# Performance work log

Hardware: AMD Instinct MI355X
Metric: run time of the kernel (lower is better)

The kernel has to match this reference:

```python
import jax, jax.numpy as jnp
import numpy as np

EPS = 1e-5


def setup_inputs() -> dict:
    key = jax.random.key(0)
    ks = jax.random.split(key, 6)
    B, N, F = 8, 8192, 64
    xyzs = jax.random.uniform(ks[0], (B, N, 3), dtype=jnp.float32)
    feats = jax.random.normal(ks[1], (B, N, F), dtype=jnp.float32)
    c_in = 3 + F  # 67
    dims = [(64, c_in), (64, 64), (128, 64)]
    inp = {"xyzs": xyzs, "feats": feats}
    for i, (co, ci) in enumerate(dims, start=1):
        inp[f"w{i}"] = jax.random.normal(ks[1 + i], (co, ci), dtype=jnp.float32) / np.sqrt(ci)
        inp[f"b{i}"] = jnp.zeros((co,), jnp.float32)
        inp[f"g{i}"] = jnp.ones((co,), jnp.float32)
        inp[f"bt{i}"] = jnp.zeros((co,), jnp.float32)
        inp[f"m{i}"] = jnp.zeros((co,), jnp.float32)
        inp[f"v{i}"] = jnp.ones((co,), jnp.float32)
    return inp


def sample_farthest_points(xyz, S):
    # Iterative FPS starting from index 0 (pytorch3d default random_start_point=False).
    B, N, _ = xyz.shape
    barange = jnp.arange(B)

    def step(carry, _):
        mind, last = carry                      # mind: [B,N] min sq-dist to selected set
        lastp = xyz[barange, last]              # [B,3]
        d = jnp.sum((xyz - lastp[:, None, :]) ** 2, -1)
        mind = jnp.minimum(mind, d)
        nxt = jnp.argmax(mind, axis=1).astype(jnp.int32)
        return (mind, nxt), nxt

    init = (jnp.full((B, N), 1e10, xyz.dtype), jnp.zeros((B,), jnp.int32))
    _, rest = jax.lax.scan(step, init, None, length=S - 1)  # [S-1, B]
    idx = jnp.concatenate([jnp.zeros((1, B), jnp.int32), rest], 0).T  # [B,S]
    return xyz[barange[:, None], idx], idx


def ball_query(centers, xyz, K, radius):
    # First-K-in-radius semantics of pytorch3d.ops.ball_query; pad idx with -1,
    # pad gathered points with zeros (masked_gather behavior).
    B, N, _ = xyz.shape
    d2 = (jnp.sum(centers ** 2, -1)[:, :, None]
          + jnp.sum(xyz ** 2, -1)[:, None, :]
          - 2.0 * jnp.einsum('bsd,bnd->bsn', centers, xyz))  # [B,S,N]
    within = d2 <= radius * radius
    skey = jnp.where(within, jnp.arange(N, dtype=jnp.int32), N)
    negvals, idx = jax.lax.top_k(-skey, K)      # K smallest keys = first K in-radius
    valid = (-negvals) < N                       # [B,S,K]
    group_idx = jnp.where(valid, idx, -1)
    gathered = xyz[jnp.arange(B)[:, None, None], jnp.where(valid, idx, 0)]  # [B,S,K,3]
    group_xyz = jnp.where(valid[..., None], gathered, 0.0)
    return group_idx, group_xyz


def _mlp_layer(x, w, b, g, bt, m, v):
    # 1x1 Conv2d over channel axis + BatchNorm (eval stats) + ReLU; x: [B,S,K,Cin]
    y = jnp.einsum('bskc,oc->bsko', x, w) + b
    y = g * (y - m) * jax.lax.rsqrt(v + EPS) + bt
    return jax.nn.relu(y)


def reference(xyzs, feats, w1, b1, g1, bt1, m1, v1,
              w2, b2, g2, bt2, m2, v2, w3, b3, g3, bt3, m3, v3):
    S, K, radius = 2048, 32, 0.2
    B = xyzs.shape[0]
    center_xyzs, _ = sample_farthest_points(xyzs, S)             # [B,S,3]
    group_idxs, group_xyzs = ball_query(center_xyzs, xyzs, K, radius)
    group_xyzs = group_xyzs - center_xyzs[:, :, None, :]          # relative coords
    batch_idxs = jnp.arange(B)[:, None, None]
    gf = feats[batch_idxs, jnp.where(group_idxs < 0, 0, group_idxs)]  # [B,S,K,F]
    gf = jnp.concatenate([group_xyzs, gf], axis=-1)
    gf = gf * (group_idxs != -1)[..., None].astype(gf.dtype)      # zero padded slots
    x = _mlp_layer(gf, w1, b1, g1, bt1, m1, v1)
    x = _mlp_layer(x, w2, b2, g2, bt2, m2, v2)
    x = _mlp_layer(x, w3, b3, g3, bt3, m3, v3)
    center_feats = jnp.max(x, axis=2)                             # max over neighbors
    return center_xyzs, center_feats
```

## Files before the change

### kernel.cpp

```cpp
#include <hip/hip_runtime.h>


#define NPTS 8192
#define SCTR 2048
#define NB   8
#define KNN  32
#define NF   64
#define WT_FLOATS (67*64 + 64*64 + 64*128)
#define PROG_STRIDE 32

typedef float v2f __attribute__((ext_vector_type(2)));

__device__ __forceinline__ v2f fps_sqdist_v2(v2f px, v2f py, v2f pz,
                                             v2f lx, v2f ly, v2f lz) {
#pragma clang fp contract(off)
  v2f dx = px - lx;
  v2f dy = py - ly;
  v2f dz = pz - lz;
  v2f xx = dx * dx;
  v2f yy = dy * dy;
  v2f zz = dz * dz;
  return (xx + yy) + zz;
}

__device__ __forceinline__ float sumsq3(float x, float y, float z) {
#pragma clang fp contract(off)
  return (x * x + y * y) + z * z;
}

__device__ __forceinline__ float bq_d2(float sc, float sx,
                                       float cx, float cy, float cz,
                                       float x, float y, float z) {
#pragma clang fp contract(off)
  float dt = fmaf(cz, z, fmaf(cy, y, cx * x));
  return (sc + sx) - 2.0f * dt;
}

template <int CTRL>
__device__ __forceinline__ unsigned long long kmax_dpp(unsigned long long k) {
  int lo = (int)(unsigned int)(k & 0xFFFFFFFFull);
  int hi = (int)(unsigned int)(k >> 32);
  int slo = __builtin_amdgcn_update_dpp(lo, lo, CTRL, 0xF, 0xF, false);
  int shi = __builtin_amdgcn_update_dpp(hi, hi, CTRL, 0xF, 0xF, false);
  unsigned long long sk =
      ((unsigned long long)(unsigned int)shi << 32) | (unsigned int)slo;
  return sk > k ? sk : k;
}

template <int CTRL>
__device__ __forceinline__ void kmax_dpp_pay(unsigned long long& k,
                                             float& x, float& y, float& z) {
  int lo = (int)(unsigned int)(k & 0xFFFFFFFFull);
  int hi = (int)(unsigned int)(k >> 32);
  int slo = __builtin_amdgcn_update_dpp(lo, lo, CTRL, 0xF, 0xF, false);
  int shi = __builtin_amdgcn_update_dpp(hi, hi, CTRL, 0xF, 0xF, false);
  int sx  = __builtin_amdgcn_update_dpp(__float_as_int(x), __float_as_int(x), CTRL, 0xF, 0xF, false);
  int sy  = __builtin_amdgcn_update_dpp(__float_as_int(y), __float_as_int(y), CTRL, 0xF, 0xF, false);
  int sz  = __builtin_amdgcn_update_dpp(__float_as_int(z), __float_as_int(z), CTRL, 0xF, 0xF, false);
  unsigned long long sk =
      ((unsigned long long)(unsigned int)shi << 32) | (unsigned int)slo;
  if (sk > k) {
    k = sk;
    x = __int_as_float(sx);
    y = __int_as_float(sy);
    z = __int_as_float(sz);
  }
}

__global__ __launch_bounds__(256) void init_kernel(
    const float* __restrict__ w1, const float* __restrict__ w2,
    const float* __restrict__ w3, float* __restrict__ wT,
    int* __restrict__ prog)
{
  const int t = threadIdx.x;
  if (blockIdx.x == 0 && t < NB) prog[t * PROG_STRIDE] = 0;
  int idx = blockIdx.x * 256 + t;
  if (idx < 67*64) {
    int c = idx >> 6, o = idx & 63;
    wT[idx] = w1[o*67 + c];
  } else if (idx < 67*64 + 64*64) {
    int r = idx - 67*64; int c = r >> 6, o = r & 63;
    wT[idx] = w2[o*64 + c];
  } else if (idx < 67*64 + 64*64 + 64*128) {
    int r = idx - (67*64 + 64*64); int c = r >> 7, o = r & 127;
    wT[idx] = w3[o*64 + c];
  }
}

__global__ __launch_bounds__(256, 1) void mega_kernel(
    const float* __restrict__ xyzs, const float* __restrict__ feats,
    float* centers, const float* __restrict__ wT, int* prog,
    const float* __restrict__ b1, const float* __restrict__ g1, const float* __restrict__ bt1,
    const float* __restrict__ m1, const float* __restrict__ v1,
    const float* __restrict__ b2, const float* __restrict__ g2, const float* __restrict__ bt2,
    const float* __restrict__ m2, const float* __restrict__ v2,
    const float* __restrict__ b3, const float* __restrict__ g3, const float* __restrict__ bt3,
    const float* __restrict__ m3, const float* __restrict__ v3,
    float* out_feats)
{
  __shared__ __align__(16) float smem[8784];

  if (blockIdx.x < NB) {
    __builtin_amdgcn_s_setprio(3);
    const int b = blockIdx.x;
    const int t = threadIdx.x;
    const int t4 = 4 * t;
    const float* xb = xyzs + (size_t)b * NPTS * 3;
    int* prog_b = prog + b * PROG_STRIDE;
    float* cb_ = centers + (size_t)b * SCTR * 3;

#define LOADQ(QX, QY, QZ, QOFF)                                               \
    { const float4* p_ = (const float4*)(xb + (size_t)3 * ((QOFF) + t4));     \
      float4 l0 = p_[0], l1 = p_[1], l2 = p_[2];                              \
      QX = make_float4(l0.x, l0.w, l1.z, l2.y);                               \
      QY = make_float4(l0.y, l1.x, l1.w, l2.z);                               \
      QZ = make_float4(l0.z, l1.y, l2.x, l2.w); }

    float4 xA, yA, zA, xB, yB, zB, xC, yC, zC, xD, yD, zD;
    float4 xE, yE, zE, xF, yF, zF, xG, yG, zG, xH, yH, zH;
    LOADQ(xA, yA, zA, 0);
    LOADQ(xB, yB, zB, 1024);
    LOADQ(xC, yC, zC, 2048);
    LOADQ(xD, yD, zD, 3072);
    LOADQ(xE, yE, zE, 4096);
    LOADQ(xF, yF, zF, 5120);
    LOADQ(xG, yG, zG, 6144);
    LOADQ(xH, yH, zH, 7168);
#undef LOADQ

    float4 mA = make_float4(1e10f, 1e10f, 1e10f, 1e10f);
    float4 mB = mA, mC = mA, mD = mA, mE = mA, mF = mA, mG = mA, mH = mA;

    if (t == 0) { smem[0] = xA.x; smem[1] = yA.x; smem[2] = zA.x; }
    __syncthreads();
    float lx = smem[0], ly = smem[1], lz = smem[2];
    if (t == 0) { cb_[0] = lx; cb_[1] = ly; cb_[2] = lz; }

#define FPS_QUAD(QX, QY, QZ, MV, QOFF, BV, BG)                                  \
  do {                                                                          \
    v2f d;                                                                      \
    d = fps_sqdist_v2((v2f){QX.x,QX.y}, (v2f){QY.x,QY.y}, (v2f){QZ.x,QZ.y},     \
                      lxv, lyv, lzv);                                           \
    MV.x = fminf(MV.x, d.x); if (MV.x > BV) { BV = MV.x; BG = (QOFF)+t4+0; }    \
    MV.y = fminf(MV.y, d.y); if (MV.y > BV) { BV = MV.y; BG = (QOFF)+t4+1; }    \
    d = fps_sqdist_v2((v2f){QX.z,QX.w}, (v2f){QY.z,QY.w}, (v2f){QZ.z,QZ.w},     \
                      lxv, lyv, lzv);                                           \
    MV.z = fminf(MV.z, d.x); if (MV.z > BV) { BV = MV.z; BG = (QOFF)+t4+2; }    \
    MV.w = fminf(MV.w, d.y); if (MV.w > BV) { BV = MV.w; BG = (QOFF)+t4+3; }    \
  } while (0)

    for (int s = 1; s < SCTR; ++s) {
      float bv0 = -1.0f, bv1 = -1.0f; int bg0 = 0, bg1 = 0;
      {
        v2f lxv = {lx, lx}, lyv = {ly, ly}, lzv = {lz, lz};
        FPS_QUAD(xA, yA, zA, mA, 0,    bv0, bg0);
        FPS_QUAD(xB, yB, zB, mB, 1024, bv0, bg0);
        FPS_QUAD(xC, yC, zC, mC, 2048, bv0, bg0);
        FPS_QUAD(xD, yD, zD, mD, 3072, bv0, bg0);
        FPS_QUAD(xE, yE, zE, mE, 4096, bv1, bg1);
        FPS_QUAD(xF, yF, zF, mF, 5120, bv1, bg1);
        FPS_QUAD(xG, yG, zG, mG, 6144, bv1, bg1);
        FPS_QUAD(xH, yH, zH, mH, 7168, bv1, bg1);
      }
      float bv = bv0; int bg = bg0;
      if (bv1 > bv0) { bv = bv1; bg = bg1; }

      unsigned long long key =
          ((unsigned long long)__float_as_uint(bv) << 13) |
          (unsigned long long)(8191 - bg);

      key = kmax_dpp<0x111>(key);
      key = kmax_dpp<0x112>(key);
      key = kmax_dpp<0x114>(key);
      key = kmax_dpp<0x118>(key);
      key = kmax_dpp<0x142>(key);
      key = kmax_dpp<0x143>(key);
      int skl = __builtin_amdgcn_readlane((int)(unsigned int)(key & 0xFFFFFFFFull), 63);
      int skh = __builtin_amdgcn_readlane((int)(unsigned int)(key >> 32), 63);
      int widx = 8191 - (skl & 0x1FFF);
      int q = widx >> 10;
      int j = widx & 3;
      int othr = (widx & 1023) >> 2;
      float wx = 0.f, wy = 0.f, wz = 0.f;
      if (t == othr) {
        float4 qx, qy, qz;
        switch (q) {
          case 0: qx = xA; qy = yA; qz = zA; break;
          case 1: qx = xB; qy = yB; qz = zB; break;
          case 2: qx = xC; qy = yC; qz = zC; break;
          case 3: qx = xD; qy = yD; qz = zD; break;
          case 4: qx = xE; qy = yE; qz = zE; break;
          case 5: qx = xF; qy = yF; qz = zF; break;
          case 6: qx = xG; qy = yG; qz = zG; break;
          default: qx = xH; qy = yH; qz = zH; break;
        }
        wx = (j == 0) ? qx.x : ((j == 1) ? qx.y : ((j == 2) ? qx.z : qx.w));
        wy = (j == 0) ? qy.x : ((j == 1) ? qy.y : ((j == 2) ? qy.z : qy.w));
        wz = (j == 0) ? qz.x : ((j == 1) ? qz.y : ((j == 2) ? qz.z : qz.w));
      }
      int ol = othr & 63;
      wx = __int_as_float(__builtin_amdgcn_readlane(__float_as_int(wx), ol));
      wy = __int_as_float(__builtin_amdgcn_readlane(__float_as_int(wy), ol));
      wz = __int_as_float(__builtin_amdgcn_readlane(__float_as_int(wz), ol));

      int pb = s & 1;
      if ((t & 63) == 63) {
        float* slot = smem + (size_t)((pb * 4 + (t >> 6)) * 8);
        slot[0] = __int_as_float(skl);
        slot[1] = __int_as_float(skh);
        slot[2] = wx; slot[3] = wy; slot[4] = wz;
      }
      __syncthreads();
      const float* rs = smem + (size_t)((pb * 4 + (t & 3)) * 8);
      unsigned long long k4 =
          ((unsigned long long)(unsigned int)__float_as_int(rs[1]) << 32) |
          (unsigned int)__float_as_int(rs[0]);
      float px = rs[2], py = rs[3], pz = rs[4];
      kmax_dpp_pay<0xB1>(k4, px, py, pz);
      kmax_dpp_pay<0x4E>(k4, px, py, pz);
      lx = px; ly = py; lz = pz;

      if (t == 0) {
        float* o = cb_ + 3 * s;
        o[0] = lx; o[1] = ly; o[2] = lz;
        if ((s & 31) == 31)
          __hip_atomic_store(prog_b, s + 1, __ATOMIC_RELEASE, __HIP_MEMORY_SCOPE_AGENT);
      }
    }
#undef FPS_QUAD
    return;
  }

  constexpr float R2 = (float)(0.2 * 0.2);
  const int t    = threadIdx.x;
  const int jb   = blockIdx.x - NB;
  const int half = t >> 7;
  const int ht   = t & 127;
  const int w    = ht >> 6;
  const int lane = ht & 63;
  const int cid  = 2 * jb + half;
  const int b    = cid & 7;
  const int s    = cid >> 3;
  const int bid  = b * SCTR + s;
  const float* xb = xyzs + (size_t)b * NPTS * 3;

  float* in_  = smem + half * 4352;
  float* y_   = in_ + 2176;
  int*   gidx = (int*)(smem + 8704) + half * KNN;
  float* csl  = smem + 8768 + half * 4;

  if (ht == 0) {
    int* pb_ = prog + b * PROG_STRIDE;
    while (__hip_atomic_load(pb_, __ATOMIC_RELAXED, __HIP_MEMORY_SCOPE_AGENT) <= s)
      __builtin_amdgcn_s_sleep(64);
    const int* cg = (const int*)(centers + (size_t)bid * 3);
    csl[0] = __int_as_float(__hip_atomic_load(cg + 0, __ATOMIC_RELAXED, __HIP_MEMORY_SCOPE_AGENT));
    csl[1] = __int_as_float(__hip_atomic_load(cg + 1, __ATOMIC_RELAXED, __HIP_MEMORY_SCOPE_AGENT));
    csl[2] = __int_as_float(__hip_atomic_load(cg + 2, __ATOMIC_RELAXED, __HIP_MEMORY_SCOPE_AGENT));
  }
  __syncthreads();
  const float cx = csl[0], cy = csl[1], cz = csl[2];
  const float sc = sumsq3(cx, cy, cz);

  int cnt = 0;
  for (int base = 0; base < NPTS && cnt < KNN; base += 64) {
    int n = base + lane;
    float x = xb[n*3+0], y = xb[n*3+1], z = xb[n*3+2];
    float sx = sumsq3(x, y, z);
    float d2 = bq_d2(sc, sx, cx, cy, cz, x, y, z);
    bool within = (d2 <= R2);
    unsigned long long mk = __ballot(within);
    int rank = __popcll(mk & ((1ull << lane) - 1ull));
    int slot = cnt + rank;
    if (within && slot < KNN) gidx[slot] = n;
    cnt += (int)__popcll(mk);
  }
  if (cnt > KNN) cnt = KNN;
  __syncthreads();

#pragma unroll 4
  for (int k2 = 0; k2 < 16; ++k2) {
    int k = 2*k2 + w;
    int gk = (k < cnt) ? gidx[k] : -1;
    float fv = 0.f, xv = 0.f;
    if (gk >= 0) {
      fv = feats[((size_t)b * NPTS + gk) * NF + lane];
      if (lane < 3) xv = xb[gk*3 + lane] - csl[lane];
    }
    in_[k*68 + 3 + lane] = fv;
    if (lane < 3) in_[k*68 + lane] = xv;
    if (lane == 3) in_[k*68 + 67] = 0.f;
  }
  __syncthreads();

  const int g  = lane >> 3;
  const int h  = lane & 7;
  const int ob = w*32 + 4*h;
  const float* w1T = wT;
  const float* w2T = wT + 67*64;
  const float* w3T = wT + 67*64 + 64*64;

#define FMA_COL(AS0, AS1, AS2, AS3, WV)                                      \
  do {                                                                       \
    acc[0][0]=fmaf(AS0, WV.x, acc[0][0]); acc[0][1]=fmaf(AS0, WV.y, acc[0][1]); \
    acc[0][2]=fmaf(AS0, WV.z, acc[0][2]); acc[0][3]=fmaf(AS0, WV.w, acc[0][3]); \
    acc[1][0]=fmaf(AS1, WV.x, acc[1][0]); acc[1][1]=fmaf(AS1, WV.y, acc[1][1]); \
    acc[1][2]=fmaf(AS1, WV.z, acc[1][2]); acc[1][3]=fmaf(AS1, WV.w, acc[1][3]); \
    acc[2][0]=fmaf(AS2, WV.x, acc[2][0]); acc[2][1]=fmaf(AS2, WV.y, acc[2][1]); \
    acc[2][2]=fmaf(AS2, WV.z, acc[2][2]); acc[2][3]=fmaf(AS2, WV.w, acc[2][3]); \
    acc[3][0]=fmaf(AS3, WV.x, acc[3][0]); acc[3][1]=fmaf(AS3, WV.y, acc[3][1]); \
    acc[3][2]=fmaf(AS3, WV.z, acc[3][2]); acc[3][3]=fmaf(AS3, WV.w, acc[3][3]); \
  } while (0)

#define MLP_CHUNK(SRC, WBASE, WSTRIDE, WOFF)                                 \
  do {                                                                       \
    float4 a0 = *(const float4*)((SRC) + (4*g+0)*68 + c0);                   \
    float4 a1 = *(const float4*)((SRC) + (4*g+1)*68 + c0);                   \
    float4 a2 = *(const float4*)((SRC) + (4*g+2)*68 + c0);                   \
    float4 a3 = *(const float4*)((SRC) + (4*g+3)*68 + c0);                   \
    float4 wv0 = *(const float4*)(WBASE + (c0+0)*(WSTRIDE) + (WOFF));        \
    float4 wv1 = *(const float4*)(WBASE + (c0+1)*(WSTRIDE) + (WOFF));        \
    float4 wv2 = *(const float4*)(WBASE + (c0+2)*(WSTRIDE) + (WOFF));        \
    float4 wv3 = *(const float4*)(WBASE + (c0+3)*(WSTRIDE) + (WOFF));        \
    FMA_COL(a0.x, a1.x, a2.x, a3.x, wv0);                                    \
    FMA_COL(a0.y, a1.y, a2.y, a3.y, wv1);                                    \
    FMA_COL(a0.z, a1.z, a2.z, a3.z, wv2);                                    \
    FMA_COL(a0.w, a1.w, a2.w, a3.w, wv3);                                    \
  } while (0)

  {
    float acc[4][4];
#pragma unroll
    for (int i=0;i<4;++i)
#pragma unroll
      for (int j=0;j<4;++j) acc[i][j]=0.f;
#pragma unroll 2
    for (int c0 = 0; c0 < 68; c0 += 4) {
      MLP_CHUNK(in_, w1T, 64, ob);
    }
    float scl[4], shf[4];
#pragma unroll
    for (int j=0;j<4;++j) {
      int o = ob + j;
      float r = g1[o] * rsqrtf(v1[o] + 1e-5f);
      scl[j] = r;
      shf[j] = (b1[o] - m1[o]) * r + bt1[o];
    }
#pragma unroll
    for (int i=0;i<4;++i) {
      float4 out;
      out.x = fmaxf(fmaf(acc[i][0], scl[0], shf[0]), 0.f);
      out.y = fmaxf(fmaf(acc[i][1], scl[1], shf[1]), 0.f);
      out.z = fmaxf(fmaf(acc[i][2], scl[2], shf[2]), 0.f);
      out.w = fmaxf(fmaf(acc[i][3], scl[3], shf[3]), 0.f);
      *(float4*)(y_ + (4*g+i)*68 + ob) = out;
    }
  }
  __syncthreads();

  {
    float acc[4][4];
#pragma unroll
    for (int i=0;i<4;++i)
#pragma unroll
      for (int j=0;j<4;++j) acc[i][j]=0.f;
#pragma unroll 2
    for (int c0 = 0; c0 < 64; c0 += 4) {
      MLP_CHUNK(y_, w2T, 64, ob);
    }
    float scl[4], shf[4];
#pragma unroll
    for (int j=0;j<4;++j) {
      int o = ob + j;
      float r = g2[o] * rsqrtf(v2[o] + 1e-5f);
      scl[j] = r;
      shf[j] = (b2[o] - m2[o]) * r + bt2[o];
    }
    __syncthreads();
#pragma unroll
    for (int i=0;i<4;++i) {
      float4 out;
      out.x = fmaxf(fmaf(acc[i][0], scl[0], shf[0]), 0.f);
      out.y = fmaxf(fmaf(acc[i][1], scl[1], shf[1]), 0.f);
      out.z = fmaxf(fmaf(acc[i][2], scl[2], shf[2]), 0.f);
      out.w = fmaxf(fmaf(acc[i][3], scl[3], shf[3]), 0.f);
      *(float4*)(in_ + (4*g+i)*68 + ob) = out;
    }
  }
  __syncthreads();

  for (int p = 0; p < 2; ++p) {
    const int o3 = w*64 + p*32 + 4*h;
    float acc[4][4];
#pragma unroll
    for (int i=0;i<4;++i)
#pragma unroll
      for (int j=0;j<4;++j) acc[i][j]=0.f;
#pragma unroll 2
    for (int c0 = 0; c0 < 64; c0 += 4) {
      MLP_CHUNK(in_, w3T, 128, o3);
    }
    float scl[4], shf[4];
#pragma unroll
    for (int j=0;j<4;++j) {
      int o = o3 + j;
      float r = g3[o] * rsqrtf(v3[o] + 1e-5f);
      scl[j] = r;
      shf[j] = (b3[o] - m3[o]) * r + bt3[o];
    }
    float vm[4];
#pragma unroll
    for (int j=0;j<4;++j) {
      float q0 = fmaxf(fmaf(acc[0][j], scl[j], shf[j]), 0.f);
      float q1 = fmaxf(fmaf(acc[1][j], scl[j], shf[j]), 0.f);
      float q2 = fmaxf(fmaf(acc[2][j], scl[j], shf[j]), 0.f);
      float q3 = fmaxf(fmaf(acc[3][j], scl[j], shf[j]), 0.f);
      vm[j] = fmaxf(fmaxf(q0,q1), fmaxf(q2,q3));
    }
#pragma unroll
    for (int mk = 8; mk < 64; mk <<= 1) {
#pragma unroll
      for (int j=0;j<4;++j) vm[j] = fmaxf(vm[j], __shfl_xor(vm[j], mk));
    }
    if (g == 0) {
      float* dst = out_feats + (size_t)bid*128 + o3;
      *(float4*)dst = make_float4(vm[0], vm[1], vm[2], vm[3]);
    }
  }
#undef MLP_CHUNK
#undef FMA_COL
}

extern "C" void kernel_launch(void* const* d_in, const int* in_sizes, int n_in,
                              void* d_out, int out_size, void* d_ws, size_t ws_size,
                              hipStream_t stream) {
  const float* xyzs  = (const float*)d_in[0];
  const float* feats = (const float*)d_in[1];
  const float* w1  = (const float*)d_in[2];
  const float* b1  = (const float*)d_in[3];
  const float* g1  = (const float*)d_in[4];
  const float* bt1 = (const float*)d_in[5];
  const float* m1  = (const float*)d_in[6];
  const float* v1  = (const float*)d_in[7];
  const float* w2  = (const float*)d_in[8];
  const float* b2  = (const float*)d_in[9];
  const float* g2  = (const float*)d_in[10];
  const float* bt2 = (const float*)d_in[11];
  const float* m2  = (const float*)d_in[12];
  const float* v2  = (const float*)d_in[13];
  const float* w3  = (const float*)d_in[14];
  const float* b3  = (const float*)d_in[15];
  const float* g3  = (const float*)d_in[16];
  const float* bt3 = (const float*)d_in[17];
  const float* m3  = (const float*)d_in[18];
  const float* v3  = (const float*)d_in[19];

  float* out       = (float*)d_out;
  float* centers   = out;
  float* out_feats = out + (size_t)NB * SCTR * 3;
  float* wT        = (float*)d_ws;
  int*   prog      = (int*)((float*)d_ws + WT_FLOATS);

  hipLaunchKernelGGL(init_kernel, dim3(65), dim3(256), 0, stream,
                     w1, w2, w3, wT, prog);
  hipLaunchKernelGGL(mega_kernel, dim3(NB + NB * SCTR / 2), dim3(256), 0, stream,
                     xyzs, feats, centers, wT, prog,
                     b1, g1, bt1, m1, v1,
                     b2, g2, bt2, m2, v2,
                     b3, g3, bt3, m3, v3,
                     out_feats);
}
```

Before: 2.386 ms.

## Use persistent worker blocks with atomic work queue and avoid CUs hosting FPS blocks

Replaces the one-block-per-center-pair grid with 1024 persistent worker blocks that take center pairs from a global atomic counter. The FPS blocks publish their hardware CU/XCC id, and any worker that lands on the same CU exits so it cannot steal issue slots from the serial FPS chain. This cuts block launch overhead and keeps waiting workers off the FPS CUs. It relies on hardware-id registers and spin-waits until all FPS blocks have registered, which risks stalls if those blocks are scheduled late.

```diff
diff --git a/kernel.cpp b/kernel.cpp
--- a/kernel.cpp
+++ b/kernel.cpp
@@ -8,6 +8,10 @@
 #define NF   64
 #define WT_FLOATS (67*64 + 64*64 + 64*128)
 #define PROG_STRIDE 32
+#define NCID (NB * SCTR)
+
+#define GETREG_HWID (4  | (31 << 11))
+#define GETREG_XCC  (20 | (31 << 11))
 
 typedef float v2f __attribute__((ext_vector_type(2)));
 
@@ -73,7 +77,7 @@
     int* __restrict__ prog)
 {
   const int t = threadIdx.x;
-  if (blockIdx.x == 0 && t < NB) prog[t * PROG_STRIDE] = 0;
+  if (blockIdx.x == 0) prog[t] = 0;
   int idx = blockIdx.x * 256 + t;
   if (idx < 67*64) {
     int c = idx >> 6, o = idx & 63;
@@ -108,6 +112,13 @@
     const float* xb = xyzs + (size_t)b * NPTS * 3;
     int* prog_b = prog + b * PROG_STRIDE;
     float* cb_ = centers + (size_t)b * SCTR * 3;
+
+    if (t == 0) {
+      unsigned hwid = (unsigned)__builtin_amdgcn_s_getreg(GETREG_HWID);
+      unsigned xcc  = (unsigned)__builtin_amdgcn_s_getreg(GETREG_XCC);
+      int mykey = (int)(((xcc & 0xFu) << 16) | (hwid & 0xFF00u)) + 1;
+      __hip_atomic_store(prog_b + 4, mykey, __ATOMIC_RELEASE, __HIP_MEMORY_SCOPE_AGENT);
+    }
 
 #define LOADQ(QX, QY, QZ, QOFF)                                               \
     { const float4* p_ = (const float4*)(xb + (size_t)3 * ((QOFF) + t4));     \
@@ -233,72 +244,102 @@
 
   constexpr float R2 = (float)(0.2 * 0.2);
   const int t    = threadIdx.x;
-  const int jb   = blockIdx.x - NB;
   const int half = t >> 7;
   const int ht   = t & 127;
   const int w    = ht >> 6;
   const int lane = ht & 63;
-  const int cid  = 2 * jb + half;
-  const int b    = cid & 7;
-  const int s    = cid >> 3;
-  const int bid  = b * SCTR + s;
-  const float* xb = xyzs + (size_t)b * NPTS * 3;
 
   float* in_  = smem + half * 4352;
   float* y_   = in_ + 2176;
   int*   gidx = (int*)(smem + 8704) + half * KNN;
   float* csl  = smem + 8768 + half * 4;
-
-  if (ht == 0) {
-    int* pb_ = prog + b * PROG_STRIDE;
-    while (__hip_atomic_load(pb_, __ATOMIC_RELAXED, __HIP_MEMORY_SCOPE_AGENT) <= s)
-      __builtin_amdgcn_s_sleep(64);
-    const int* cg = (const int*)(centers + (size_t)bid * 3);
-    csl[0] = __int_as_float(__hip_atomic_load(cg + 0, __ATOMIC_RELAXED, __HIP_MEMORY_SCOPE_AGENT));
-    csl[1] = __int_as_float(__hip_atomic_load(cg + 1, __ATOMIC_RELAXED, __HIP_MEMORY_SCOPE_AGENT));
-    csl[2] = __int_as_float(__hip_atomic_load(cg + 2, __ATOMIC_RELAXED, __HIP_MEMORY_SCOPE_AGENT));
+  int*   shint = (int*)(smem + 8776);
+
+  if (t == 0) {
+    unsigned hwid = (unsigned)__builtin_amdgcn_s_getreg(GETREG_HWID);
+    unsigned xcc  = (unsigned)__builtin_amdgcn_s_getreg(GETREG_XCC);
+    int mykey = (int)(((xcc & 0xFu) << 16) | (hwid & 0xFF00u)) + 1;
+    int col;
+    for (;;) {
+      int seen = 0; col = 0;
+      for (int bb = 0; bb < NB; ++bb) {
+        int kk = __hip_atomic_load(prog + bb * PROG_STRIDE + 4,
+                                   __ATOMIC_RELAXED, __HIP_MEMORY_SCOPE_AGENT);
+        seen += (kk != 0);
+        col  |= (kk == mykey);
+      }
+      if (seen == NB) break;
+      __builtin_amdgcn_s_sleep(16);
+    }
+    shint[0] = col;
   }
   __syncthreads();
-  const float cx = csl[0], cy = csl[1], cz = csl[2];
-  const float sc = sumsq3(cx, cy, cz);
-
-  int cnt = 0;
-  for (int base = 0; base < NPTS && cnt < KNN; base += 64) {
-    int n = base + lane;
-    float x = xb[n*3+0], y = xb[n*3+1], z = xb[n*3+2];
-    float sx = sumsq3(x, y, z);
-    float d2 = bq_d2(sc, sx, cx, cy, cz, x, y, z);
-    bool within = (d2 <= R2);
-    unsigned long long mk = __ballot(within);
-    int rank = __popcll(mk & ((1ull << lane) - 1ull));
-    int slot = cnt + rank;
-    if (within && slot < KNN) gidx[slot] = n;
-    cnt += (int)__popcll(mk);
-  }
-  if (cnt > KNN) cnt = KNN;
+  const int colocated = shint[0];
   __syncthreads();
+  if (colocated) return;
+
+  for (;;) {
+    if (t == 0) shint[0] = atomicAdd(prog + 8, 2);
+    __syncthreads();
+    const int base = shint[0];
+    if (base >= NCID) break;
+    int cid = base + half;
+    if (cid > NCID - 1) cid = NCID - 1;
+    const int b   = cid & 7;
+    const int s   = cid >> 3;
+    const int bid = b * SCTR + s;
+    const float* xb = xyzs + (size_t)b * NPTS * 3;
+
+    if (ht == 0) {
+      int* pb_ = prog + b * PROG_STRIDE;
+      while (__hip_atomic_load(pb_, __ATOMIC_RELAXED, __HIP_MEMORY_SCOPE_AGENT) <= s)
+        __builtin_amdgcn_s_sleep(64);
+      const int* cg = (const int*)(centers + (size_t)bid * 3);
+      csl[0] = __int_as_float(__hip_atomic_load(cg + 0, __ATOMIC_RELAXED, __HIP_MEMORY_SCOPE_AGENT));
+      csl[1] = __int_as_float(__hip_atomic_load(cg + 1, __ATOMIC_RELAXED, __HIP_MEMORY_SCOPE_AGENT));
+      csl[2] = __int_as_float(__hip_atomic_load(cg + 2, __ATOMIC_RELAXED, __HIP_MEMORY_SCOPE_AGENT));
+    }
+    __syncthreads();
+    const float cx = csl[0], cy = csl[1], cz = csl[2];
+    const float sc = sumsq3(cx, cy, cz);
+
+    int cnt = 0;
+    for (int bs = 0; bs < NPTS && cnt < KNN; bs += 64) {
+      int n = bs + lane;
+      float x = xb[n*3+0], y = xb[n*3+1], z = xb[n*3+2];
+      float sx = sumsq3(x, y, z);
+      float d2 = bq_d2(sc, sx, cx, cy, cz, x, y, z);
+      bool within = (d2 <= R2);
+      unsigned long long mk = __ballot(within);
+      int rank = __popcll(mk & ((1ull << lane) - 1ull));
+      int slot = cnt + rank;
+      if (within && slot < KNN) gidx[slot] = n;
+      cnt += (int)__popcll(mk);
+    }
+    if (cnt > KNN) cnt = KNN;
+    __syncthreads();
 
 #pragma unroll 4
-  for (int k2 = 0; k2 < 16; ++k2) {
-    int k = 2*k2 + w;
-    int gk = (k < cnt) ? gidx[k] : -1;
-    float fv = 0.f, xv = 0.f;
-    if (gk >= 0) {
-      fv = feats[((size_t)b * NPTS + gk) * NF + lane];
-      if (lane < 3) xv = xb[gk*3 + lane] - csl[lane];
-    }
-    in_[k*68 + 3 + lane] = fv;
-    if (lane < 3) in_[k*68 + lane] = xv;
-    if (lane == 3) in_[k*68 + 67] = 0.f;
-  }
-  __syncthreads();
-
-  const int g  = lane >> 3;
-  const int h  = lane & 7;
-  const int ob = w*32 + 4*h;
-  const float* w1T = wT;
-  const float* w2T = wT + 67*64;
-  const float* w3T = wT + 67*64 + 64*64;
+    for (int k2 = 0; k2 < 16; ++k2) {
+      int k = 2*k2 + w;
+      int gk = (k < cnt) ? gidx[k] : -1;
+      float fv = 0.f, xv = 0.f;
+      if (gk >= 0) {
+        fv = feats[((size_t)b * NPTS + gk) * NF + lane];
+        if (lane < 3) xv = xb[gk*3 + lane] - csl[lane];
+      }
+      in_[k*68 + 3 + lane] = fv;
+      if (lane < 3) in_[k*68 + lane] = xv;
+      if (lane == 3) in_[k*68 + 67] = 0.f;
+    }
+    __syncthreads();
+
+    const int g  = lane >> 3;
+    const int h  = lane & 7;
+    const int ob = w*32 + 4*h;
+    const float* w1T = wT;
+    const float* w2T = wT + 67*64;
+    const float* w3T = wT + 67*64 + 64*64;
 
 #define FMA_COL(AS0, AS1, AS2, AS3, WV)                                      \
   do {                                                                       \
@@ -328,107 +369,110 @@
     FMA_COL(a0.w, a1.w, a2.w, a3.w, wv3);                                    \
   } while (0)
 
-  {
-    float acc[4][4];
-#pragma unroll
-    for (int i=0;i<4;++i)
-#pragma unroll
-      for (int j=0;j<4;++j) acc[i][j]=0.f;
+    {
+      float acc[4][4];
+#pragma unroll
+      for (int i=0;i<4;++i)
+#pragma unroll
+        for (int j=0;j<4;++j) acc[i][j]=0.f;
 #pragma unroll 2
-    for (int c0 = 0; c0 < 68; c0 += 4) {
-      MLP_CHUNK(in_, w1T, 64, ob);
-    }
-    float scl[4], shf[4];
-#pragma unroll
-    for (int j=0;j<4;++j) {
-      int o = ob + j;
-      float r = g1[o] * rsqrtf(v1[o] + 1e-5f);
-      scl[j] = r;
-      shf[j] = (b1[o] - m1[o]) * r + bt1[o];
-    }
-#pragma unroll
-    for (int i=0;i<4;++i) {
-      float4 out;
-      out.x = fmaxf(fmaf(acc[i][0], scl[0], shf[0]), 0.f);
-      out.y = fmaxf(fmaf(acc[i][1], scl[1], shf[1]), 0.f);
-      out.z = fmaxf(fmaf(acc[i][2], scl[2], shf[2]), 0.f);
-      out.w = fmaxf(fmaf(acc[i][3], scl[3], shf[3]), 0.f);
-      *(float4*)(y_ + (4*g+i)*68 + ob) = out;
-    }
-  }
-  __syncthreads();
-
-  {
-    float acc[4][4];
-#pragma unroll
-    for (int i=0;i<4;++i)
-#pragma unroll
-      for (int j=0;j<4;++j) acc[i][j]=0.f;
+      for (int c0 = 0; c0 < 68; c0 += 4) {
+        MLP_CHUNK(in_, w1T, 64, ob);
+      }
+      float scl[4], shf[4];
+#pragma unroll
+      for (int j=0;j<4;++j) {
+        int o = ob + j;
+        float r = g1[o] * rsqrtf(v1[o] + 1e-5f);
+        scl[j] = r;
+        shf[j] = (b1[o] - m1[o]) * r + bt1[o];
+      }
+#pragma unroll
+      for (int i=0;i<4;++i) {
+        float4 out;
+        out.x = fmaxf(fmaf(acc[i][0], scl[0], shf[0]), 0.f);
+        out.y = fmaxf(fmaf(acc[i][1], scl[1], shf[1]), 0.f);
+        out.z = fmaxf(fmaf(acc[i][2], scl[2], shf[2]), 0.f);
+        out.w = fmaxf(fmaf(acc[i][3], scl[3], shf[3]), 0.f);
+        *(float4*)(y_ + (4*g+i)*68 + ob) = out;
+      }
+    }
+    __syncthreads();
+
+    {
+      float acc[4][4];
+#pragma unroll
+      for (int i=0;i<4;++i)
+#pragma unroll
+        for (int j=0;j<4;++j) acc[i][j]=0.f;
 #pragma unroll 2
-    for (int c0 = 0; c0 < 64; c0 += 4) {
-      MLP_CHUNK(y_, w2T, 64, ob);
-    }
-    float scl[4], shf[4];
-#pragma unroll
-    for (int j=0;j<4;++j) {
-      int o = ob + j;
-      float r = g2[o] * rsqrtf(v2[o] + 1e-5f);
-      scl[j] = r;
-      shf[j] = (b2[o] - m2[o]) * r + bt2[o];
-    }
-    __syncthreads();
-#pragma unroll
-    for (int i=0;i<4;++i) {
-      float4 out;
-      out.x = fmaxf(fmaf(acc[i][0], scl[0], shf[0]), 0.f);
-      out.y = fmaxf(fmaf(acc[i][1], scl[1], shf[1]), 0.f);
-      out.z = fmaxf(fmaf(acc[i][2], scl[2], shf[2]), 0.f);
-      out.w = fmaxf(fmaf(acc[i][3], scl[3], shf[3]), 0.f);
-      *(float4*)(in_ + (4*g+i)*68 + ob) = out;
-    }
-  }
-  __syncthreads();
-
-  for (int p = 0; p < 2; ++p) {
-    const int o3 = w*64 + p*32 + 4*h;
-    float acc[4][4];
-#pragma unroll
-    for (int i=0;i<4;++i)
-#pragma unroll
-      for (int j=0;j<4;++j) acc[i][j]=0.f;
+      for (int c0 = 0; c0 < 64; c0 += 4) {
+        MLP_CHUNK(y_, w2T, 64, ob);
+      }
+      float scl[4], shf[4];
+#pragma unroll
+      for (int j=0;j<4;++j) {
+        int o = ob + j;
+        float r = g2[o] * rsqrtf(v2[o] + 1e-5f);
+        scl[j] = r;
+        shf[j] = (b2[o] - m2[o]) * r + bt2[o];
+      }
+      __syncthreads();
+#pragma unroll
+      for (int i=0;i<4;++i) {
+        float4 out;
+        out.x = fmaxf(fmaf(acc[i][0], scl[0], shf[0]), 0.f);
+        out.y = fmaxf(fmaf(acc[i][1], scl[1], shf[1]), 0.f);
+        out.z = fmaxf(fmaf(acc[i][2], scl[2], shf[2]), 0.f);
+        out.w = fmaxf(fmaf(acc[i][3], scl[3], shf[3]), 0.f);
+        *(float4*)(in_ + (4*g+i)*68 + ob) = out;
+      }
+    }
+    __syncthreads();
+
+    for (int p = 0; p < 2; ++p) {
+      const int o3 = w*64 + p*32 + 4*h;
+      float acc[4][4];
+#pragma unroll
+      for (int i=0;i<4;++i)
+#pragma unroll
+        for (int j=0;j<4;++j) acc[i][j]=0.f;
 #pragma unroll 2
-    for (int c0 = 0; c0 < 64; c0 += 4) {
-      MLP_CHUNK(in_, w3T, 128, o3);
-    }
-    float scl[4], shf[4];
-#pragma unroll
-    for (int j=0;j<4;++j) {
-      int o = o3 + j;
-      float r = g3[o] * rsqrtf(v3[o] + 1e-5f);
-      scl[j] = r;
-      shf[j] = (b3[o] - m3[o]) * r + bt3[o];
-    }
-    float vm[4];
-#pragma unroll
-    for (int j=0;j<4;++j) {
-      float q0 = fmaxf(fmaf(acc[0][j], scl[j], shf[j]), 0.f);
-      float q1 = fmaxf(fmaf(acc[1][j], scl[j], shf[j]), 0.f);
-      float q2 = fmaxf(fmaf(acc[2][j], scl[j], shf[j]), 0.f);
-      float q3 = fmaxf(fmaf(acc[3][j], scl[j], shf[j]), 0.f);
-      vm[j] = fmaxf(fmaxf(q0,q1), fmaxf(q2,q3));
-    }
-#pragma unroll
-    for (int mk = 8; mk < 64; mk <<= 1) {
-#pragma unroll
-      for (int j=0;j<4;++j) vm[j] = fmaxf(vm[j], __shfl_xor(vm[j], mk));
-    }
-    if (g == 0) {
-      float* dst = out_feats + (size_t)bid*128 + o3;
-      *(float4*)dst = make_float4(vm[0], vm[1], vm[2], vm[3]);
-    }
-  }
+      for (int c0 = 0; c0 < 64; c0 += 4) {
+        MLP_CHUNK(in_, w3T, 128, o3);
+      }
+      float scl[4], shf[4];
+#pragma unroll
+      for (int j=0;j<4;++j) {
+        int o = o3 + j;
+        float r = g3[o] * rsqrtf(v3[o] + 1e-5f);
+        scl[j] = r;
+        shf[j] = (b3[o] - m3[o]) * r + bt3[o];
+      }
+      float vm[4];
+#pragma unroll
+      for (int j=0;j<4;++j) {
+        float q0 = fmaxf(fmaf(acc[0][j], scl[j], shf[j]), 0.f);
+        float q1 = fmaxf(fmaf(acc[1][j], scl[j], shf[j]), 0.f);
+        float q2 = fmaxf(fmaf(acc[2][j], scl[j], shf[j]), 0.f);
+        float q3 = fmaxf(fmaf(acc[3][j], scl[j], shf[j]), 0.f);
+        vm[j] = fmaxf(fmaxf(q0,q1), fmaxf(q2,q3));
+      }
+#pragma unroll
+      for (int mk = 8; mk < 64; mk <<= 1) {
+#pragma unroll
+        for (int j=0;j<4;++j) vm[j] = fmaxf(vm[j], __shfl_xor(vm[j], mk));
+      }
+      if (g == 0) {
+        float* dst = out_feats + (size_t)bid*128 + o3;
+        *(float4*)dst = make_float4(vm[0], vm[1], vm[2], vm[3]);
+      }
+    }
 #undef MLP_CHUNK
 #undef FMA_COL
+
+    __syncthreads();
+  }
 }
 
 extern "C" void kernel_launch(void* const* d_in, const int* in_sizes, int n_in,
@@ -463,7 +507,7 @@
 
   hipLaunchKernelGGL(init_kernel, dim3(65), dim3(256), 0, stream,
                      w1, w2, w3, wT, prog);
-  hipLaunchKernelGGL(mega_kernel, dim3(NB + NB * SCTR / 2), dim3(256), 0, stream,
+  hipLaunchKernelGGL(mega_kernel, dim3(NB + 1024), dim3(256), 0, stream,
                      xyzs, feats, centers, wT, prog,
                      b1, g1, bt1, m1, v1,
                      b2, g2, bt2, m2, v2,
```

Result: no change. 2.422 ms (+1.5%).
